# Kernel optimization log

Hardware: AMD Instinct MI355X
Metric: run time of the kernel (lower is better)

Reference implementation:

```python
import jax, jax.numpy as jnp
import numpy as np

N_EMBD = 1024
N_HEAD = 16
B, T = 4, 2048


def setup_inputs() -> dict:
    key = jax.random.key(0)
    ks = jax.random.split(key, 5)
    s_in = 1.0 / np.sqrt(N_EMBD)
    return {
        "x": jax.random.normal(ks[0], (B, T, N_EMBD), dtype=jnp.float32),
        "W_qkv": jax.random.normal(ks[1], (N_EMBD, 3 * N_EMBD), dtype=jnp.float32) * s_in,
        "b_qkv": jnp.zeros((3 * N_EMBD,), dtype=jnp.float32),
        "W_proj": jax.random.normal(ks[2], (N_EMBD, N_EMBD), dtype=jnp.float32) * s_in,
        "b_proj": jnp.zeros((N_EMBD,), dtype=jnp.float32),
    }


def reference(x, W_qkv, b_qkv, W_proj, b_proj):
    Bx, Tx, C = x.shape
    hd = C // N_HEAD
    qkv = x @ W_qkv + b_qkv                      # [B,T,3C]
    q, k, v = jnp.split(qkv, 3, axis=2)

    def rs(t):
        return t.reshape(Bx, Tx, N_HEAD, hd).transpose(0, 2, 1, 3)  # [B,H,T,hd]

    q, k, v = rs(q), rs(k), rs(v)
    scale = 1.0 / np.sqrt(hd)
    attn = jnp.einsum('bhqd,bhkd->bhqk', q, k) * scale
    causal = jnp.tril(jnp.ones((Tx, Tx), dtype=bool))
    attn = jnp.where(causal[None, None], attn, -jnp.inf)
    attn = jax.nn.softmax(attn, axis=-1)
    out = jnp.einsum('bhqk,bhkd->bhqd', attn, v)
    out = out.transpose(0, 2, 1, 3).reshape(Bx, Tx, C)
    return out @ W_proj + b_proj
```

## Files before the change

kernel.cpp:

```cpp
#include <hip/hip_runtime.h>
#include <hip/hip_bf16.h>

typedef __attribute__((ext_vector_type(8))) short short8;
typedef __attribute__((ext_vector_type(4))) float f32x4;

#define QSCALE 0.1803368801111204f

__device__ inline unsigned short f2b(float f){
  union { float f; unsigned int u; } a; a.f = f;
  unsigned int u = a.u;
  unsigned int r = (u + 0x7fff + ((u >> 16) & 1)) >> 16;
  return (unsigned short)r;
}

__device__ inline unsigned short f2brn(float f){
  __hip_bfloat16 h = __float2bfloat16(f);
  union { __hip_bfloat16 h; unsigned short u; } c; c.h = h;
  return c.u;
}

__device__ inline void gload16(const unsigned short* g, unsigned short* l){
  __builtin_amdgcn_global_load_lds((const __attribute__((address_space(1))) void*)g,
                                   (__attribute__((address_space(3))) void*)l, 16, 0, 0);
}

__global__ void k_cast_x(const float* __restrict__ x, unsigned short* __restrict__ xb, int n4){
  int i = blockIdx.x * blockDim.x + threadIdx.x;
  if (i < n4){
    float4 v = ((const float4*)x)[i];
    ushort4 o;
    o.x = f2b(v.x); o.y = f2b(v.y); o.z = f2b(v.z); o.w = f2b(v.w);
    ((ushort4*)xb)[i] = o;
  }
}

__global__ void k_transpose_cast(const float* __restrict__ in, unsigned short* __restrict__ out,
                                 int R, int Cc){
  __shared__ float tile[32][33];
  int bx = blockIdx.x, by = blockIdx.y;
  int tx = threadIdx.x, ty = threadIdx.y;
  int col = bx*32 + tx;
  #pragma unroll
  for (int jj = 0; jj < 4; ++jj){
    int row = by*32 + ty + jj*8;
    tile[ty + jj*8][tx] = in[(size_t)row*Cc + col];
  }
  __syncthreads();
  int r = by*32 + tx;
  #pragma unroll
  for (int jj = 0; jj < 4; ++jj){
    int c = bx*32 + ty + jj*8;
    out[(size_t)c*R + r] = f2b(tile[tx][ty + jj*8]);
  }
}

template<int MODE>
__global__ __launch_bounds__(256) void k_gemm_bt(
    const unsigned short* __restrict__ A,
    const unsigned short* __restrict__ Bt,
    const float* __restrict__ bias,
    float* __restrict__ Cout,
    unsigned short* __restrict__ qb,
    unsigned short* __restrict__ kbf,
    unsigned short* __restrict__ vbf,
    int Mdim, int Ndim, int Kdim)
{
  __shared__ alignas(16) unsigned short As[3*128*32];
  __shared__ alignas(16) unsigned short Bs[3*128*32];
  const int tid  = threadIdx.x;
  const int lane = tid & 63;
  const int wid  = tid >> 6;
  const int wm   = wid >> 1, wn = wid & 1;
  const int bn   = blockIdx.x, bm = blockIdx.y;
  const int l15  = lane & 15, lhi = lane >> 4;

  f32x4 acc[4][4] = {};

  const int rowA0 = bm * 128, rowB0 = bn * 128;
  const unsigned short* Ag = A  + (size_t)(rowA0 + (tid>>2)) * Kdim + (tid&3)*8;
  const unsigned short* Bg = Bt + (size_t)(rowB0 + (tid>>2)) * Kdim + (tid&3)*8;
  const size_t row64 = (size_t)64 * Kdim;

  const int nK = Kdim >> 5;

#define G_STAGE(t, b) do {                                   \
    const int _ko = (t)*32;                                  \
    unsigned short* _as = As + (b)*4096;                     \
    unsigned short* _bs = Bs + (b)*4096;                     \
    gload16(Ag + _ko,         _as + tid*8);                  \
    gload16(Ag + row64 + _ko, _as + 2048 + tid*8);           \
    gload16(Bg + _ko,         _bs + tid*8);                  \
    gload16(Bg + row64 + _ko, _bs + 2048 + tid*8);           \
  } while(0)

  G_STAGE(0, 0);
  G_STAGE(1, 1);

  int cb = 0, sb = 2;
  for (int kt = 0; kt < nK; ++kt){
    asm volatile("s_waitcnt vmcnt(4)" ::: "memory");
    __builtin_amdgcn_s_barrier();
    if (kt + 2 < nK) G_STAGE(kt + 2, sb);
    const unsigned short* Ac = As + cb*4096;
    const unsigned short* Bc = Bs + cb*4096;
    short8 af[4], bfr[4];
    #pragma unroll
    for (int f = 0; f < 4; ++f){
      af[f]  = *(const short8*)(Ac + (wm*64 + f*16 + l15)*32 + lhi*8);
      bfr[f] = *(const short8*)(Bc + (wn*64 + f*16 + l15)*32 + lhi*8);
    }
    __builtin_amdgcn_s_setprio(1);
    #pragma unroll
    for (int fm = 0; fm < 4; ++fm)
      #pragma unroll
      for (int fn = 0; fn < 4; ++fn)
        acc[fm][fn] = __builtin_amdgcn_mfma_f32_16x16x32_bf16(af[fm], bfr[fn], acc[fm][fn], 0, 0, 0);
    __builtin_amdgcn_s_setprio(0);
    cb = (cb == 2) ? 0 : cb + 1;
    sb = (sb == 2) ? 0 : sb + 1;
  }
#undef G_STAGE

  #pragma unroll
  for (int fm = 0; fm < 4; ++fm){
    #pragma unroll
    for (int fn = 0; fn < 4; ++fn){
      #pragma unroll
      for (int j = 0; j < 4; ++j){
        int m = bm*128 + wm*64 + fm*16 + lhi*4 + j;
        int n = bn*128 + wn*64 + fn*16 + l15;
        float v = acc[fm][fn][j] + bias[n];
        if (MODE == 0){
          int which = n >> 10; int cc2 = n & 1023; int h = cc2 >> 6; int d = cc2 & 63;
          int bb = m >> 11;    int t = m & 2047;
          if (which == 2){
            vbf[((size_t)(bb*16 + h)*64 + d)*2048 + t] = f2b(v);
          } else {
            if (which == 0) v *= QSCALE;
            unsigned short* dst = (which == 0) ? qb : kbf;
            dst[(size_t)((bb*16 + h)*2048 + t)*64 + d] = f2b(v);
          }
        } else {
          Cout[(size_t)m * Ndim + n] = v;
        }
      }
    }
  }
}

__global__ __launch_bounds__(256) void k_attn(
    const unsigned short* __restrict__ qb,
    const unsigned short* __restrict__ kbuf,
    const unsigned short* __restrict__ vT,
    unsigned short* __restrict__ ao)
{
  __shared__ alignas(16) unsigned short K_lds[3*64*64];
  __shared__ alignas(16) unsigned short V_lds[3*64*64];
  __shared__ alignas(16) unsigned short P_lds[4*32*72];
  const int tid  = threadIdx.x;
  const int lane = tid & 63, wid = tid >> 6;
  const int l15  = lane & 15, lhi = lane >> 4;
  const int qt   = (int)gridDim.x - 1 - (int)blockIdx.x;
  const int bh   = blockIdx.y;
  const size_t base = (size_t)bh * 2048 * 64;
  const int q0w  = qt*128 + wid*32;
  const int qmaxw = q0w + 31;

  const int sr  = tid >> 3;
  const int sck = (tid & 7) ^ (sr & 7);
  const unsigned short* kg0 = kbuf + base + (size_t)(sr     )*64 + sck*8;
  const unsigned short* kg1 = kbuf + base + (size_t)(sr + 32)*64 + sck*8;
  const unsigned short* vg0 = vT   + base + (size_t)(sr     )*2048 + sck*8;
  const unsigned short* vg1 = vT   + base + (size_t)(sr + 32)*2048 + sck*8;

#define A_STAGE(t, b) do {                                   \
    const int _kb = (t)*64;                                  \
    unsigned short* _kd = K_lds + (b)*4096;                  \
    unsigned short* _vd = V_lds + (b)*4096;                  \
    gload16(kg0 + (size_t)_kb*64, _kd + tid*8);              \
    gload16(kg1 + (size_t)_kb*64, _kd + 2048 + tid*8);       \
    gload16(vg0 + _kb,            _vd + tid*8);              \
    gload16(vg1 + _kb,            _vd + 2048 + tid*8);       \
  } while(0)

  short8 qf[2][2];
  #pragma unroll
  for (int g = 0; g < 2; ++g)
    #pragma unroll
    for (int i = 0; i < 2; ++i)
      qf[g][i] = *(const short8*)(qb + base + (size_t)(q0w + g*16 + l15)*64 + i*32 + lhi*8);

  float m_run[2] = {-1e30f, -1e30f};
  float l_run[2] = {0.f, 0.f};
  f32x4 o_acc[2][4] = {};
  unsigned short* Pw = P_lds + wid*32*72;

  const int nkt = 2*qt + 2;

  A_STAGE(0, 0);
  A_STAGE(1, 1);

  int cb = 0, sb = 2;
  for (int kt = 0; kt < nkt; ++kt){
    asm volatile("s_waitcnt vmcnt(4)" ::: "memory");
    __builtin_amdgcn_s_barrier();
    if (kt + 2 < nkt) A_STAGE(kt + 2, sb);
    if (kt*64 <= qmaxw){
      const unsigned short* Kc = K_lds + cb*4096;
      const unsigned short* Vc = V_lds + cb*4096;
      short8 kf[4][2];
      #pragma unroll
      for (int fn = 0; fn < 4; ++fn)
        #pragma unroll
        for (int i = 0; i < 2; ++i)
          kf[fn][i] = *(const short8*)(Kc + (fn*16 + l15)*64 + (((i*4 + lhi) ^ (l15 & 7)) << 3));
      f32x4 s[2][4] = {};
      __builtin_amdgcn_s_setprio(1);
      #pragma unroll
      for (int g = 0; g < 2; ++g)
        #pragma unroll
        for (int fn = 0; fn < 4; ++fn)
          #pragma unroll
          for (int i = 0; i < 2; ++i)
            s[g][fn] = __builtin_amdgcn_mfma_f32_16x16x32_bf16(kf[fn][i], qf[g][i], s[g][fn], 0, 0, 0);
      __builtin_amdgcn_s_setprio(0);
      if (kt >= 2*qt){
        #pragma unroll
        for (int g = 0; g < 2; ++g){
          const int qi = q0w + g*16 + l15;
          #pragma unroll
          for (int fn = 0; fn < 4; ++fn)
            #pragma unroll
            for (int j = 0; j < 4; ++j){
              int ki = kt*64 + fn*16 + lhi*4 + j;
              if (ki > qi) s[g][fn][j] = -1e30f;
            }
        }
      }
      float rmax[2];
      #pragma unroll
      for (int g = 0; g < 2; ++g){
        float t0 = fmaxf(fmaxf(s[g][0][0], s[g][0][1]), fmaxf(s[g][0][2], s[g][0][3]));
        float t1 = fmaxf(fmaxf(s[g][1][0], s[g][1][1]), fmaxf(s[g][1][2], s[g][1][3]));
        float t2 = fmaxf(fmaxf(s[g][2][0], s[g][2][1]), fmaxf(s[g][2][2], s[g][2][3]));
        float t3 = fmaxf(fmaxf(s[g][3][0], s[g][3][1]), fmaxf(s[g][3][2], s[g][3][3]));
        float v = fmaxf(fmaxf(t0, t1), fmaxf(t2, t3));
        v = fmaxf(v, __shfl_xor(v, 16));
        v = fmaxf(v, __shfl_xor(v, 32));
        rmax[g] = v;
      }
      bool need = (rmax[0] > m_run[0] + 8.f) || (rmax[1] > m_run[1] + 8.f);
      if (__any(need)){
        #pragma unroll
        for (int g = 0; g < 2; ++g){
          float mn   = fmaxf(m_run[g], rmax[g]);
          float corr = exp2f(m_run[g] - mn);
          m_run[g] = mn;
          l_run[g] *= corr;
          #pragma unroll
          for (int j = 0; j < 4; ++j){
            float cj = __shfl(corr, (lane & 48) | (lhi*4 + j));
            #pragma unroll
            for (int df = 0; df < 4; ++df) o_acc[g][df][j] *= cj;
          }
        }
      }
      #pragma unroll
      for (int g = 0; g < 2; ++g){
        const float mr = m_run[g];
        float rsum = 0.f;
        unsigned long long pwq[4];
        #pragma unroll
        for (int fn = 0; fn < 4; ++fn){
          float e0 = exp2f(s[g][fn][0] - mr);
          float e1 = exp2f(s[g][fn][1] - mr);
          float e2 = exp2f(s[g][fn][2] - mr);
          float e3 = exp2f(s[g][fn][3] - mr);
          rsum += (e0 + e1) + (e2 + e3);
          unsigned int w0 = (unsigned int)f2brn(e0) | ((unsigned int)f2brn(e1) << 16);
          unsigned int w1 = (unsigned int)f2brn(e2) | ((unsigned int)f2brn(e3) << 16);
          pwq[fn] = (unsigned long long)w0 | ((unsigned long long)w1 << 32);
        }
        rsum += __shfl_xor(rsum, 16);
        rsum += __shfl_xor(rsum, 32);
        l_run[g] += rsum;
        #pragma unroll
        for (int fn = 0; fn < 4; ++fn)
          *(unsigned long long*)(Pw + (g*16 + l15)*72 + fn*16 + lhi*4) = pwq[fn];
      }
      short8 pa[2][2];
      #pragma unroll
      for (int g = 0; g < 2; ++g)
        #pragma unroll
        for (int i = 0; i < 2; ++i)
          pa[g][i] = *(const short8*)(Pw + (g*16 + l15)*72 + i*32 + lhi*8);
      __builtin_amdgcn_s_setprio(1);
      #pragma unroll
      for (int df = 0; df < 4; ++df){
        #pragma unroll
        for (int i = 0; i < 2; ++i){
          short8 vf = *(const short8*)(Vc + (df*16 + l15)*64 + (((i*4 + lhi) ^ (l15 & 7)) << 3));
          #pragma unroll
          for (int g = 0; g < 2; ++g)
            o_acc[g][df] = __builtin_amdgcn_mfma_f32_16x16x32_bf16(pa[g][i], vf, o_acc[g][df], 0, 0, 0);
        }
      }
      __builtin_amdgcn_s_setprio(0);
    }
    cb = (cb == 2) ? 0 : cb + 1;
    sb = (sb == 2) ? 0 : sb + 1;
  }
#undef A_STAGE
  const int b = bh >> 4, h = bh & 15;
  #pragma unroll
  for (int g = 0; g < 2; ++g){
    float rln = 1.0f / l_run[g];
    #pragma unroll
    for (int j = 0; j < 4; ++j){
      float rl = __shfl(rln, (lane & 48) | (lhi*4 + j));
      int qrow = q0w + g*16 + lhi*4 + j;
      #pragma unroll
      for (int df = 0; df < 4; ++df){
        float v = o_acc[g][df][j] * rl;
        ao[(size_t)(b*2048 + qrow)*1024 + h*64 + df*16 + l15] = f2brn(v);
      }
    }
  }
}

extern "C" void kernel_launch(void* const* d_in, const int* in_sizes, int n_in,
                              void* d_out, int out_size, void* d_ws, size_t ws_size,
                              hipStream_t stream){
  const float* x     = (const float*)d_in[0];
  const float* Wqkv  = (const float*)d_in[1];
  const float* bqkv  = (const float*)d_in[2];
  const float* Wproj = (const float*)d_in[3];
  const float* bproj = (const float*)d_in[4];
  float* out = (float*)d_out;

  unsigned short* ws     = (unsigned short*)d_ws;
  unsigned short* xb     = ws;
  unsigned short* wqkvT  = xb + 8388608;
  unsigned short* wprojT = wqkvT + 3145728;
  unsigned short* qbuf   = wprojT + 1048576;
  unsigned short* kbuf   = qbuf + 8388608;
  unsigned short* vbuf   = kbuf + 8388608;
  unsigned short* ao     = vbuf + 8388608;

  k_cast_x<<<8192, 256, 0, stream>>>(x, xb, 2097152);
  k_transpose_cast<<<dim3(96, 32), dim3(32, 8), 0, stream>>>(Wqkv, wqkvT, 1024, 3072);
  k_transpose_cast<<<dim3(32, 32), dim3(32, 8), 0, stream>>>(Wproj, wprojT, 1024, 1024);
  k_gemm_bt<0><<<dim3(24, 64), 256, 0, stream>>>(xb, wqkvT, bqkv, nullptr,
                                                 qbuf, kbuf, vbuf, 8192, 3072, 1024);
  k_attn<<<dim3(16, 64), 256, 0, stream>>>(qbuf, kbuf, vbuf, ao);
  k_gemm_bt<1><<<dim3(8, 64), 256, 0, stream>>>(ao, wprojT, bproj, out,
                                                nullptr, nullptr, nullptr, 8192, 1024, 1024);
}
```

Measured before the change: 385.3 us.

## Use double-buffered KV staging, register-shuffle P transpose, and packed V stores

The attention kernel moves from a triple-buffered K/V LDS pipeline to double buffering, issuing each prefetch at the top of the iteration and adding a trailing barrier. The P tile now goes from accumulator layout to operand layout through cross-lane shuffles instead of an LDS round-trip, and the P LDS buffer is removed. The GEMM epilogue hoists the bias load and writes the transposed V output as packed 64-bit stores. The GEMM also waits for all outstanding loads on its last iteration. The aim is to cut LDS traffic and footprint, which may allow more resident blocks. The cost is an extra barrier per tile and less prefetch depth.

Measured after the change: 368.5 us. 1.05x faster.

```diff
diff --git a/kernel.cpp b/kernel.cpp
--- a/kernel.cpp
+++ b/kernel.cpp
@@ -22,6 +22,12 @@
 __device__ inline void gload16(const unsigned short* g, unsigned short* l){
   __builtin_amdgcn_global_load_lds((const __attribute__((address_space(1))) void*)g,
                                    (__attribute__((address_space(3))) void*)l, 16, 0, 0);
+}
+
+__device__ inline unsigned long long shfl64(unsigned long long v, int src){
+  int lo = __shfl((int)(unsigned)(v & 0xffffffffull), src);
+  int hi = __shfl((int)(unsigned)(v >> 32), src);
+  return ((unsigned long long)(unsigned)hi << 32) | (unsigned)(unsigned int)lo;
 }
 
 __global__ void k_cast_x(const float* __restrict__ x, unsigned short* __restrict__ xb, int n4){
@@ -98,7 +104,8 @@
 
   int cb = 0, sb = 2;
   for (int kt = 0; kt < nK; ++kt){
-    asm volatile("s_waitcnt vmcnt(4)" ::: "memory");
+    if (kt + 1 < nK) { asm volatile("s_waitcnt vmcnt(4)" ::: "memory"); }
+    else             { asm volatile("s_waitcnt vmcnt(0)" ::: "memory"); }
     __builtin_amdgcn_s_barrier();
     if (kt + 2 < nK) G_STAGE(kt + 2, sb);
     const unsigned short* Ac = As + cb*4096;
@@ -125,24 +132,33 @@
   for (int fm = 0; fm < 4; ++fm){
     #pragma unroll
     for (int fn = 0; fn < 4; ++fn){
-      #pragma unroll
-      for (int j = 0; j < 4; ++j){
-        int m = bm*128 + wm*64 + fm*16 + lhi*4 + j;
-        int n = bn*128 + wn*64 + fn*16 + l15;
-        float v = acc[fm][fn][j] + bias[n];
-        if (MODE == 0){
-          int which = n >> 10; int cc2 = n & 1023; int h = cc2 >> 6; int d = cc2 & 63;
-          int bb = m >> 11;    int t = m & 2047;
-          if (which == 2){
-            vbf[((size_t)(bb*16 + h)*64 + d)*2048 + t] = f2b(v);
-          } else {
+      int n  = bn*128 + wn*64 + fn*16 + l15;
+      int m0 = bm*128 + wm*64 + fm*16 + lhi*4;
+      if (MODE == 0){
+        int which = n >> 10; int cc2 = n & 1023; int h = cc2 >> 6; int d = cc2 & 63;
+        int bb = m0 >> 11;   int t0 = m0 & 2047;
+        if (which == 2){
+          float bv = bias[n];
+          unsigned long long pk = 0;
+          #pragma unroll
+          for (int j = 0; j < 4; ++j)
+            pk |= (unsigned long long)f2b(acc[fm][fn][j] + bv) << (16*j);
+          *(unsigned long long*)(vbf + ((size_t)(bb*16 + h)*64 + d)*2048 + t0) = pk;
+        } else {
+          unsigned short* dst = (which == 0) ? qb : kbf;
+          float bv = bias[n];
+          #pragma unroll
+          for (int j = 0; j < 4; ++j){
+            float v = acc[fm][fn][j] + bv;
             if (which == 0) v *= QSCALE;
-            unsigned short* dst = (which == 0) ? qb : kbf;
-            dst[(size_t)((bb*16 + h)*2048 + t)*64 + d] = f2b(v);
+            dst[(size_t)((bb*16 + h)*2048 + t0 + j)*64 + d] = f2b(v);
           }
-        } else {
-          Cout[(size_t)m * Ndim + n] = v;
-        }
+        }
+      } else {
+        float bv = bias[n];
+        #pragma unroll
+        for (int j = 0; j < 4; ++j)
+          Cout[(size_t)(m0 + j) * Ndim + n] = acc[fm][fn][j] + bv;
       }
     }
   }
@@ -154,9 +170,8 @@
     const unsigned short* __restrict__ vT,
     unsigned short* __restrict__ ao)
 {
-  __shared__ alignas(16) unsigned short K_lds[3*64*64];
-  __shared__ alignas(16) unsigned short V_lds[3*64*64];
-  __shared__ alignas(16) unsigned short P_lds[4*32*72];
+  __shared__ alignas(16) unsigned short K_lds[2*64*64];
+  __shared__ alignas(16) unsigned short V_lds[2*64*64];
   const int tid  = threadIdx.x;
   const int lane = tid & 63, wid = tid >> 6;
   const int l15  = lane & 15, lhi = lane >> 4;
@@ -193,21 +208,28 @@
   float m_run[2] = {-1e30f, -1e30f};
   float l_run[2] = {0.f, 0.f};
   f32x4 o_acc[2][4] = {};
-  unsigned short* Pw = P_lds + wid*32*72;
 
   const int nkt = 2*qt + 2;
 
+  const int bs = ((lhi & 1) << 1) | (lhi >> 1);
+  const int sA = l15 + (bs << 4);
+  const int sB = l15 + ((bs ^ 1) << 4);
+  const bool selodd = (lhi & 1);
+  const bool lowh   = (lhi < 2);
+
   A_STAGE(0, 0);
-  A_STAGE(1, 1);
-
-  int cb = 0, sb = 2;
+
   for (int kt = 0; kt < nkt; ++kt){
-    asm volatile("s_waitcnt vmcnt(4)" ::: "memory");
+    if (kt + 1 < nkt){
+      A_STAGE(kt + 1, (kt + 1) & 1);
+      asm volatile("s_waitcnt vmcnt(4)" ::: "memory");
+    } else {
+      asm volatile("s_waitcnt vmcnt(0)" ::: "memory");
+    }
     __builtin_amdgcn_s_barrier();
-    if (kt + 2 < nkt) A_STAGE(kt + 2, sb);
     if (kt*64 <= qmaxw){
-      const unsigned short* Kc = K_lds + cb*4096;
-      const unsigned short* Vc = V_lds + cb*4096;
+      const unsigned short* Kc = K_lds + (kt & 1)*4096;
+      const unsigned short* Vc = V_lds + (kt & 1)*4096;
       short8 kf[4][2];
       #pragma unroll
       for (int fn = 0; fn < 4; ++fn)
@@ -265,11 +287,11 @@
           }
         }
       }
+      unsigned long long pwq[2][4];
       #pragma unroll
       for (int g = 0; g < 2; ++g){
         const float mr = m_run[g];
         float rsum = 0.f;
-        unsigned long long pwq[4];
         #pragma unroll
         for (int fn = 0; fn < 4; ++fn){
           float e0 = exp2f(s[g][fn][0] - mr);
@@ -279,21 +301,28 @@
           rsum += (e0 + e1) + (e2 + e3);
           unsigned int w0 = (unsigned int)f2brn(e0) | ((unsigned int)f2brn(e1) << 16);
           unsigned int w1 = (unsigned int)f2brn(e2) | ((unsigned int)f2brn(e3) << 16);
-          pwq[fn] = (unsigned long long)w0 | ((unsigned long long)w1 << 32);
+          pwq[g][fn] = (unsigned long long)w0 | ((unsigned long long)w1 << 32);
         }
         rsum += __shfl_xor(rsum, 16);
         rsum += __shfl_xor(rsum, 32);
         l_run[g] += rsum;
-        #pragma unroll
-        for (int fn = 0; fn < 4; ++fn)
-          *(unsigned long long*)(Pw + (g*16 + l15)*72 + fn*16 + lhi*4) = pwq[fn];
       }
       short8 pa[2][2];
       #pragma unroll
-      for (int g = 0; g < 2; ++g)
-        #pragma unroll
-        for (int i = 0; i < 2; ++i)
-          pa[g][i] = *(const short8*)(Pw + (g*16 + l15)*72 + i*32 + lhi*8);
+      for (int g = 0; g < 2; ++g){
+        unsigned long long pubA0 = selodd ? pwq[g][1] : pwq[g][0];
+        unsigned long long pubB0 = selodd ? pwq[g][0] : pwq[g][1];
+        unsigned long long pubA1 = selodd ? pwq[g][3] : pwq[g][2];
+        unsigned long long pubB1 = selodd ? pwq[g][2] : pwq[g][3];
+        unsigned long long rA0 = shfl64(pubA0, sA);
+        unsigned long long rB0 = shfl64(pubB0, sB);
+        unsigned long long rA1 = shfl64(pubA1, sA);
+        unsigned long long rB1 = shfl64(pubB1, sB);
+        union { unsigned long long q[2]; short8 v; } u0, u1;
+        u0.q[0] = lowh ? rA0 : rB0;  u0.q[1] = lowh ? rB0 : rA0;
+        u1.q[0] = lowh ? rA1 : rB1;  u1.q[1] = lowh ? rB1 : rA1;
+        pa[g][0] = u0.v;  pa[g][1] = u1.v;
+      }
       __builtin_amdgcn_s_setprio(1);
       #pragma unroll
       for (int df = 0; df < 4; ++df){
@@ -307,8 +336,7 @@
       }
       __builtin_amdgcn_s_setprio(0);
     }
-    cb = (cb == 2) ? 0 : cb + 1;
-    sb = (sb == 2) ? 0 : sb + 1;
+    __builtin_amdgcn_s_barrier();
   }
 #undef A_STAGE
   const int b = bh >> 4, h = bh & 15;
```
